# Performance work log

Measured on AMD Instinct MI355X. Metric: run time of the kernel, lower is better.

Reference implementation:

```python
import jax, jax.numpy as jnp
import numpy as np

N_HEADS = 32
N_KV_HEADS = 8
HEAD_DIM = 64
ROPE_BASE = 10000.0


def setup_inputs() -> dict:
    key = jax.random.key(0)
    ks = jax.random.split(key, 5)
    B, T, C = 4, 1024, 2048
    kv_dim = N_KV_HEADS * HEAD_DIM
    scale = 0.02
    return {
        "x": jax.random.normal(ks[0], (B, T, C), dtype=jnp.float32),
        "Wq": jax.random.normal(ks[1], (C, C), dtype=jnp.float32) * scale,
        "Wk": jax.random.normal(ks[2], (C, kv_dim), dtype=jnp.float32) * scale,
        "Wv": jax.random.normal(ks[3], (C, kv_dim), dtype=jnp.float32) * scale,
        "Wp": jax.random.normal(ks[4], (C, C), dtype=jnp.float32) * scale,
    }


def _rotate_half(x):
    # interleaved rotation: (x0,x1,x2,x3,...) -> (-x1,x0,-x3,x2,...)
    x1 = x[..., ::2]
    x2 = x[..., 1::2]
    return jnp.stack((-x2, x1), axis=-1).reshape(x.shape)


def _rope_tables(T, dtype):
    inv_freq = 1.0 / (ROPE_BASE ** (jnp.arange(0, HEAD_DIM, 2, dtype=jnp.float32) / HEAD_DIM))
    freqs = jnp.arange(T, dtype=jnp.float32)[:, None] * inv_freq[None, :]  # (T, D/2)
    cos = jnp.repeat(jnp.cos(freqs), 2, axis=-1).astype(dtype)  # (T, D)
    sin = jnp.repeat(jnp.sin(freqs), 2, axis=-1).astype(dtype)
    return cos[None, None], sin[None, None]  # (1,1,T,D)


def reference(x, Wq, Wk, Wv, Wp):
    B, T, C = x.shape
    H, KV, D = N_HEADS, N_KV_HEADS, HEAD_DIM
    q = (x @ Wq).reshape(B, T, H, D).transpose(0, 2, 1, 3)   # (B,H,T,D)
    k = (x @ Wk).reshape(B, T, KV, D).transpose(0, 2, 1, 3)  # (B,KV,T,D)
    v = (x @ Wv).reshape(B, T, KV, D).transpose(0, 2, 1, 3)

    cos, sin = _rope_tables(T, x.dtype)
    q = q * cos + _rotate_half(q) * sin
    k = k * cos + _rotate_half(k) * sin

    rf = H // KV
    k = jnp.repeat(k, rf, axis=1)  # (B,H,T,D) GQA broadcast
    v = jnp.repeat(v, rf, axis=1)

    scores = jnp.einsum('bhqd,bhkd->bhqk', q, k) / jnp.sqrt(jnp.asarray(D, x.dtype))
    causal = jnp.tril(jnp.ones((T, T), dtype=bool))
    scores = jnp.where(causal[None, None], scores, -jnp.inf)
    attn = jax.nn.softmax(scores, axis=-1)
    out = jnp.einsum('bhqk,bhkd->bhqd', attn, v)  # (B,H,T,D)
    out = out.transpose(0, 2, 1, 3).reshape(B, T, C)
    return out @ Wp
```

## Files before the change

kernel.cpp:

```cpp
#include <hip/hip_runtime.h>
#include <hip/hip_bf16.h>


typedef __attribute__((ext_vector_type(4))) float f32x4;
typedef __attribute__((ext_vector_type(8))) short short8;

#define AS1C(p) ((const __attribute__((address_space(1))) void*)(p))
#define AS3(p)  ((__attribute__((address_space(3))) void*)(p))

__device__ __forceinline__ unsigned short f2bf(float f) {
  union { float f; unsigned int u; } x; x.f = f;
  unsigned int r = x.u + 0x7FFFu + ((x.u >> 16) & 1u);
  return (unsigned short)(r >> 16);
}

__device__ __forceinline__ unsigned short bfc(float f) {
  return __bfloat16_as_ushort(__float2bfloat16(f));
}

__device__ __forceinline__ float ex2(float x) {
  return __builtin_amdgcn_exp2f(x);
}

__global__ void rope_tab_kernel(float2* __restrict__ tab) {
  const int idx = blockIdx.x * 256 + threadIdx.x;
  const int t = idx >> 5, i = idx & 31;
  const float invf = exp2f(-(float)i * 0.41524101186092029f);
  float sv, cv;
  __sincosf((float)t * invf, &sv, &cv);
  tab[idx] = make_float2(cv, sv);
}

__global__ void cvt_bf16_kernel(const float* __restrict__ src,
                                unsigned short* __restrict__ dst, int n4) {
  int i = blockIdx.x * blockDim.x + threadIdx.x;
  if (i >= n4) return;
  const f32x4 v = *(const f32x4*)(src + (size_t)i * 4);
  ushort4 u = make_ushort4(f2bf(v[0]), f2bf(v[1]), f2bf(v[2]), f2bf(v[3]));
  *(ushort4*)(dst + (size_t)i * 4) = u;
}

__global__ void transpose_qkv_w_kernel(const float* __restrict__ Wq,
                                       const float* __restrict__ Wk,
                                       const float* __restrict__ Wv,
                                       unsigned short* __restrict__ dst) {
  __shared__ float tile[32][33];
  const int z = blockIdx.z;
  const float* src;
  int N, rowOff;
  float scale;
  if (z == 0)      { src = Wq; N = 2048; rowOff = 0;    scale = 0.18033688011112042f; }
  else if (z == 1) { src = Wk; N = 512;  rowOff = 2048; scale = 1.0f; }
  else             { src = Wv; N = 512;  rowOff = 2560; scale = 1.0f; }
  const int n0 = blockIdx.x * 32, k0 = blockIdx.y * 32;
  if (n0 >= N) return;
  const int tx = threadIdx.x & 31, ty = threadIdx.x >> 5;
#pragma unroll
  for (int i = ty; i < 32; i += 8)
    tile[i][tx] = src[(size_t)(k0 + i) * N + (n0 + tx)];
  __syncthreads();
#pragma unroll
  for (int i = ty; i < 32; i += 8)
    dst[(size_t)(rowOff + n0 + i) * 2048 + (k0 + tx)] = f2bf(tile[tx][i] * scale);
}

__global__ void transpose_bf16_kernel(const float* __restrict__ src,
                                      unsigned short* __restrict__ dst,
                                      int N, int rowOff, float scale) {
  __shared__ float tile[32][33];
  const int n0 = blockIdx.x * 32, k0 = blockIdx.y * 32;
  const int tx = threadIdx.x & 31, ty = threadIdx.x >> 5;
#pragma unroll
  for (int i = ty; i < 32; i += 8)
    tile[i][tx] = src[(size_t)(k0 + i) * N + (n0 + tx)];
  __syncthreads();
#pragma unroll
  for (int i = ty; i < 32; i += 8)
    dst[(size_t)(rowOff + n0 + i) * 2048 + (k0 + tx)] = f2bf(tile[tx][i] * scale);
}

__global__ void rope_cvt2_kernel(const float2* __restrict__ tab,
                                 const float* __restrict__ qkf,
                                 unsigned short* __restrict__ qb,
                                 unsigned short* __restrict__ kb) {
  const int idx = blockIdx.x * 256 + threadIdx.x;
  const int m = idx / 320;
  const int p = idx - m * 320;
  const int t = m & 1023;
  unsigned short* dst;
  int srcCol, dcol;
  if (p < 256) { dcol = p * 8; srcCol = dcol; dst = qb + (size_t)m * 2048 + dcol; }
  else         { dcol = (p - 256) * 8; srcCol = 2048 + dcol; dst = kb + (size_t)m * 512 + dcol; }
  const int i0 = (srcCol & 63) >> 1;
  const float* src = qkf + (size_t)m * 2560 + srcCol;
  const f32x4 v0 = *(const f32x4*)(src);
  const f32x4 v1 = *(const f32x4*)(src + 4);
  float x[8] = {v0[0], v0[1], v0[2], v0[3], v1[0], v1[1], v1[2], v1[3]};
  short8 o;
#pragma unroll
  for (int j = 0; j < 4; ++j) {
    const float2 cs = tab[t * 32 + i0 + j];
    const float x1 = x[2 * j], x2 = x[2 * j + 1];
    o[2 * j]     = (short)bfc(x1 * cs.x - x2 * cs.y);
    o[2 * j + 1] = (short)bfc(x2 * cs.x + x1 * cs.y);
  }
  *(short8*)dst = o;
}

#define BAR() __builtin_amdgcn_s_barrier()

#define SA3(tile, half)                                                                  \
  do {                                                                                   \
    const unsigned short* p_ = Ap + (size_t)(m0 + (half) * 128 + sr) * 2048 + (tile) * 64 + sc; \
    const int d_ = (((tile) & 1) << 14) + ((half) << 13) + tid * 8;                      \
    __builtin_amdgcn_global_load_lds(AS1C(p_), AS3(&S[d_]), 16, 0, 0);                   \
    __builtin_amdgcn_global_load_lds(AS1C(p_ + (size_t)64 * 2048), AS3(&S[d_ + 4096]), 16, 0, 0); \
  } while (0)

#define SB3(tile, u)                                                                     \
  do {                                                                                   \
    const unsigned short* p_ = Bp + (size_t)(n0 + (u) * 64 + sr) * 2048 + (tile) * 64 + sc; \
    const int d_ = 32768 + ((tile) & 1) * 12288 + (u) * 4096 + tid * 8;                  \
    __builtin_amdgcn_global_load_lds(AS1C(p_), AS3(&S[d_]), 16, 0, 0);                   \
  } while (0)

#define RDA3(tile)                                                                       \
  _Pragma("unroll") for (int kk = 0; kk < 2; ++kk)                                       \
  _Pragma("unroll") for (int fm = 0; fm < 4; ++fm) {                                     \
    const int r_ = mg * 64 + fm * 16 + l15;                                              \
    af[kk][fm] = *(const short8*)&S[(((tile) & 1) << 14) + r_ * 64 +                     \
                                    (((kk << 2) | lg) ^ (r_ & 7)) * 8];                  \
  }

#define RDB3(tile, p)                                                                    \
  _Pragma("unroll") for (int kk = 0; kk < 2; ++kk)                                       \
  _Pragma("unroll") for (int jj = 0; jj < 2; ++jj) {                                     \
    const int r_ = ng * 96 + ((p) * 2 + jj) * 16 + l15;                                  \
    bf[kk][jj] = *(const short8*)&S[32768 + ((tile) & 1) * 12288 + r_ * 64 +             \
                                    (((kk << 2) | lg) ^ (r_ & 7)) * 8];                  \
  }

#define MM3(p)                                                                           \
  do {                                                                                   \
    __builtin_amdgcn_s_setprio(1);                                                       \
    _Pragma("unroll") for (int kk = 0; kk < 2; ++kk)                                     \
    _Pragma("unroll") for (int fm = 0; fm < 4; ++fm)                                     \
    _Pragma("unroll") for (int jj = 0; jj < 2; ++jj)                                     \
      acc[fm][(p) * 2 + jj] = __builtin_amdgcn_mfma_f32_16x16x32_bf16(                   \
          af[kk][fm], bf[kk][jj], acc[fm][(p) * 2 + jj], 0, 0, 0);                       \
    __builtin_amdgcn_s_setprio(0);                                                       \
  } while (0)

__global__ __launch_bounds__(512, 1) void gemm256x192_qkv_kernel(
    const unsigned short* __restrict__ Ap, const unsigned short* __restrict__ Bp,
    float* __restrict__ qkf, unsigned short* __restrict__ vt) {
  __shared__ unsigned short S[57344];
  const int tid = threadIdx.x;
  const int lane = tid & 63, w = tid >> 6;
  const int l15 = lane & 15, lg = lane >> 4;
  int lid = blockIdx.x + 16 * blockIdx.y;
  lid = (lid & 7) * 32 + (lid >> 3);
  const int m0 = (lid >> 4) * 256, n0 = (lid & 15) * 192;
  const int mg = w >> 1;
  const int ng = w & 1;
  const int sr = tid >> 3;
  const int sc = ((tid & 7) ^ (sr & 7)) << 3;
  const int NT = 32;

  f32x4 acc[4][6];
#pragma unroll
  for (int i = 0; i < 4; ++i)
#pragma unroll
    for (int j = 0; j < 6; ++j)
#pragma unroll
      for (int c = 0; c < 4; ++c) acc[i][j][c] = 0.f;

  SA3(0, 0); SA3(0, 1); SB3(0, 0); SB3(0, 1); SB3(0, 2);
  SA3(1, 0); SA3(1, 1); SB3(1, 0);
  asm volatile("s_waitcnt vmcnt(5)" ::: "memory");
  BAR();

  short8 af[2][4], bf[2][2];

  for (int t = 0; t < NT; t += 2) {
    const bool nl = (t + 2 < NT);
    RDA3(t); RDB3(t, 0);
    SB3(t + 1, 1); SB3(t + 1, 2);
    BAR();
    MM3(0);
    BAR();
    RDB3(t, 1);
    if (nl) SA3(t + 2, 0);
    BAR();
    MM3(1);
    BAR();
    RDB3(t, 2);
    if (nl) {
      SA3(t + 2, 1); SB3(t + 2, 0);
      asm volatile("s_waitcnt vmcnt(5)" ::: "memory");
    } else {
      asm volatile("s_waitcnt vmcnt(0)" ::: "memory");
    }
    BAR();
    MM3(2);
    BAR();
    RDA3(t + 1); RDB3(t + 1, 0);
    if (nl) { SB3(t + 2, 1); SB3(t + 2, 2); }
    BAR();
    MM3(0);
    BAR();
    RDB3(t + 1, 1);
    if (nl) SA3(t + 3, 0);
    BAR();
    MM3(1);
    BAR();
    RDB3(t + 1, 2);
    if (nl) {
      SA3(t + 3, 1); SB3(t + 3, 0);
      asm volatile("s_waitcnt vmcnt(5)" ::: "memory");
    }
    BAR();
    MM3(2);
    BAR();
  }

#pragma unroll
  for (int fn = 0; fn < 6; ++fn) {
    const int col16 = n0 + ng * 96 + fn * 16;
    if (col16 < 2560) {
#pragma unroll
      for (int fm = 0; fm < 4; ++fm) {
        const int row = m0 + mg * 64 + fm * 16 + lg * 4;
        const size_t base = (size_t)row * 2560 + col16 + l15;
#pragma unroll
        for (int r = 0; r < 4; ++r) qkf[base + (size_t)r * 2560] = acc[fm][fn][r];
      }
    } else {
      const int dz = (col16 - 2560) >> 6;
      const int d = ((col16 - 2560) & 63) + l15;
#pragma unroll
      for (int fm = 0; fm < 4; ++fm) {
        const int row = m0 + mg * 64 + fm * 16 + lg * 4;
        const int z = (row >> 10) * 8 + dz;
        const int t0 = row & 1023;
        ushort4 u = make_ushort4(bfc(acc[fm][fn][0]), bfc(acc[fm][fn][1]),
                                 bfc(acc[fm][fn][2]), bfc(acc[fm][fn][3]));
        *(ushort4*)&vt[(size_t)z * 65536 + d * 1024 + t0] = u;
      }
    }
  }
}

#define SA2(tile, half)                                                                  \
  do {                                                                                   \
    const unsigned short* p_ = Ap + (size_t)(m0 + (half) * 128 + sr) * Kd + (tile) * 64 + sc; \
    const int d_ = (((tile) & 1) << 14) + ((half) << 13) + tid * 8;                      \
    __builtin_amdgcn_global_load_lds(AS1C(p_), AS3(&S[d_]), 16, 0, 0);                   \
    __builtin_amdgcn_global_load_lds(AS1C(p_ + (size_t)64 * Kd), AS3(&S[d_ + 4096]), 16, 0, 0); \
  } while (0)

#define SB2(tile)                                                                        \
  do {                                                                                   \
    const unsigned short* p_ = Bp + (size_t)(n0 + sr) * Kd + (tile) * 64 + sc;           \
    const int d_ = 32768 + (((tile) & 1) << 13) + tid * 8;                               \
    __builtin_amdgcn_global_load_lds(AS1C(p_), AS3(&S[d_]), 16, 0, 0);                   \
    __builtin_amdgcn_global_load_lds(AS1C(p_ + (size_t)64 * Kd), AS3(&S[d_ + 4096]), 16, 0, 0); \
  } while (0)

#define RDA2(tile, Msub)                                                                 \
  _Pragma("unroll") for (int kk = 0; kk < 2; ++kk)                                       \
  _Pragma("unroll") for (int fm = 0; fm < 4; ++fm) {                                     \
    const int r_ = (Msub) * 64 + fm * 16 + l15;                                          \
    af[kk][fm] = *(const short8*)&S[(((tile) & 1) << 14) + (ah << 13) + r_ * 64 +        \
                                    (((kk << 2) | lg) ^ (r_ & 7)) * 8];                  \
  }

#define RDB2(dst, tile)                                                                  \
  _Pragma("unroll") for (int kk = 0; kk < 2; ++kk)                                       \
  _Pragma("unroll") for (int j = 0; j < 2; ++j) {                                        \
    const int r_ = wn + j * 16 + l15;                                                    \
    dst[kk][j] = *(const short8*)&S[32768 + (((tile) & 1) << 13) + r_ * 64 +             \
                                    (((kk << 2) | lg) ^ (r_ & 7)) * 8];                  \
  }

#define MM2(Msub, bb)                                                                    \
  do {                                                                                   \
    __builtin_amdgcn_s_setprio(1);                                                       \
    _Pragma("unroll") for (int kk = 0; kk < 2; ++kk)                                     \
    _Pragma("unroll") for (int fm = 0; fm < 4; ++fm)                                     \
    _Pragma("unroll") for (int j = 0; j < 2; ++j)                                        \
      acc[(Msub) * 4 + fm][j] = __builtin_amdgcn_mfma_f32_16x16x32_bf16(                 \
          af[kk][fm], bb[kk][j], acc[(Msub) * 4 + fm][j], 0, 0, 0);                      \
    __builtin_amdgcn_s_setprio(0);                                                       \
  } while (0)

__global__ __launch_bounds__(512, 1) void gemm256x128_kernel(
    const unsigned short* __restrict__ Ap, const unsigned short* __restrict__ Bp,
    float* __restrict__ C, int K, int N) {
  __shared__ unsigned short S[49152];
  const int tid = threadIdx.x;
  const int lane = tid & 63, w = tid >> 6;
  const int l15 = lane & 15, lg = lane >> 4;
  const int nwgx = gridDim.x;
  const int nwg = nwgx * gridDim.y;
  int lid = blockIdx.x + nwgx * blockIdx.y;
  lid = (lid & 7) * (nwg >> 3) + (lid >> 3);
  const int m0 = (lid / nwgx) * 256, n0 = (lid % nwgx) * 128;
  const int ah = w >> 2;
  const int wn = (w & 3) * 32;
  const int NT = K >> 6;
  const int Kd = K;
  const int sr = tid >> 3;
  const int sc = ((tid & 7) ^ (sr & 7)) << 3;

  f32x4 acc[8][2];
#pragma unroll
  for (int i = 0; i < 8; ++i)
#pragma unroll
    for (int j = 0; j < 2; ++j)
#pragma unroll
      for (int c = 0; c < 4; ++c) acc[i][j][c] = 0.f;

  SB2(0); SA2(0, 0); SA2(0, 1); SB2(1); SA2(1, 0);
  asm volatile("s_waitcnt vmcnt(4)" ::: "memory");
  __builtin_amdgcn_s_barrier();

  short8 af[2][4], b0[2][2], b1[2][2];

  for (int t = 0; t < NT; t += 2) {
    const bool nl = (t + 2 < NT);
    RDA2(t, 0); RDB2(b0, t);
    SA2(t + 1, 1);
    BAR();
    MM2(0, b0);
    BAR();
    RDA2(t, 1);
    if (nl) {
      SB2(t + 2); SA2(t + 2, 0);
      asm volatile("s_waitcnt vmcnt(4)" ::: "memory");
    } else {
      asm volatile("s_waitcnt vmcnt(0)" ::: "memory");
    }
    BAR();
    MM2(1, b0);
    BAR();
    RDA2(t + 1, 0); RDB2(b1, t + 1);
    if (nl) SA2(t + 2, 1);
    BAR();
    MM2(0, b1);
    BAR();
    RDA2(t + 1, 1);
    if (nl) {
      SB2(t + 3); SA2(t + 3, 0);
      asm volatile("s_waitcnt vmcnt(4)" ::: "memory");
    }
    BAR();
    MM2(1, b1);
    BAR();
  }

#pragma unroll
  for (int fm8 = 0; fm8 < 8; ++fm8)
#pragma unroll
    for (int j = 0; j < 2; ++j) {
      const size_t base =
          (size_t)(m0 + ah * 128 + (fm8 >> 2) * 64 + (fm8 & 3) * 16 + lg * 4) * N +
          (n0 + wn + j * 16 + l15);
#pragma unroll
      for (int r = 0; r < 4; ++r) C[base + (size_t)r * N] = acc[fm8][j][r];
    }
}

__global__ __launch_bounds__(256) void attn_mfma_kernel(
    const unsigned short* __restrict__ qb, const unsigned short* __restrict__ kb,
    const unsigned short* __restrict__ vt, unsigned short* __restrict__ attnb) {
  int lid = blockIdx.x + 8 * (blockIdx.y + 32 * blockIdx.z);
  lid = (lid & 7) * 128 + (lid >> 3);
  const int bx = lid & 7, h = (lid >> 3) & 31, b = lid >> 8;
  const int kvh = h >> 2;
  __shared__ unsigned short S[20480];
  const int tid = threadIdx.x, lane = tid & 63, w = tid >> 6;
  const int l15 = lane & 15, lg = lane >> 4;
  const int rowbase = w * 16 + lg * 4;

  const int gi0 = w * 64 + lane;
  const int r0 = gi0 >> 3, g0 = (gi0 & 7) ^ (r0 & 7);
  const int gi1 = (4 + w) * 64 + lane;
  const int r1 = gi1 >> 3, g1 = (gi1 & 7) ^ (r1 & 7);

  const unsigned short* kbase = kb + (size_t)b * 1024 * 512 + kvh * 64;
  const unsigned short* vbase = vt + (size_t)(b * 8 + kvh) * 64 * 1024;

#define STAGE_KV(kOff, vOff, jj)                                                    \
  do {                                                                              \
    __builtin_amdgcn_global_load_lds(AS1C(kbase + ((jj) * 64 + r0) * 512 + g0 * 8), \
                                     AS3(&S[(kOff) + w * 512]), 16, 0, 0);          \
    __builtin_amdgcn_global_load_lds(AS1C(kbase + ((jj) * 64 + r1) * 512 + g1 * 8), \
                                     AS3(&S[(kOff) + (4 + w) * 512]), 16, 0, 0);    \
    __builtin_amdgcn_global_load_lds(AS1C(vbase + r0 * 1024 + (jj) * 64 + g0 * 8),  \
                                     AS3(&S[(vOff) + w * 512]), 16, 0, 0);          \
    __builtin_amdgcn_global_load_lds(AS1C(vbase + r1 * 1024 + (jj) * 64 + g1 * 8),  \
                                     AS3(&S[(vOff) + (4 + w) * 512]), 16, 0, 0);    \
  } while (0)

#define STAGE_Q(qt)                                                                     \
  do {                                                                                  \
    const size_t qr_ = (size_t)b * 1024 + (qt) * 64;                                    \
    __builtin_amdgcn_global_load_lds(AS1C(qb + (qr_ + r0) * 2048 + h * 64 + g0 * 8),    \
                                     AS3(&S[w * 512]), 16, 0, 0);                       \
    __builtin_amdgcn_global_load_lds(AS1C(qb + (qr_ + r1) * 2048 + h * 64 + g1 * 8),    \
                                     AS3(&S[(4 + w) * 512]), 16, 0, 0);                 \
  } while (0)

  const int qts0 = bx, qts1 = 15 - bx;

  short8 ones;
#pragma unroll
  for (int i = 0; i < 8; ++i) ones[i] = (short)0x3F80;

  STAGE_Q(qts0);
  STAGE_KV(4096, 12288, 0);
  __syncthreads();

  int g = 0;
  for (int sub = 0; sub < 2; ++sub) {
    const int qtc = sub ? qts1 : qts0;
    const size_t qrow0 = (size_t)b * 1024 + qtc * 64;

    short8 qf[2];
#pragma unroll
    for (int kk = 0; kk < 2; ++kk) {
      const int r = w * 16 + l15;
      const int gq = ((kk << 2) | lg) ^ (r & 7);
      qf[kk] = *(const short8*)&S[r * 64 + gq * 8];
    }

    f32x4 oa[4], oe;
#pragma unroll
    for (int r = 0; r < 4; ++r) oe[r] = 0.f;
#pragma unroll
    for (int fd = 0; fd < 4; ++fd)
#pragma unroll
      for (int r = 0; r < 4; ++r) oa[fd][r] = 0.f;

    for (int j = 0; j <= qtc; ++j, ++g) {
      const int cur = g & 1;
      const int kOff = 4096 + cur * 4096;
      const int vOff = 12288 + cur * 4096;
      if (g < 16) {
        const int nj = (g + 1 <= qts0) ? g + 1 : g - qts0;
        STAGE_KV(4096 + (cur ^ 1) * 4096, 12288 + (cur ^ 1) * 4096, nj);
      }

      f32x4 sa[4];
#pragma unroll
      for (int fn = 0; fn < 4; ++fn)
#pragma unroll
        for (int r = 0; r < 4; ++r) sa[fn][r] = 0.f;
#pragma unroll
      for (int kk = 0; kk < 2; ++kk) {
        short8 kf[4];
#pragma unroll
        for (int fn = 0; fn < 4; ++fn) {
          const int rkv = fn * 16 + l15;
          const int gk = ((kk << 2) | lg) ^ (rkv & 7);
          kf[fn] = *(const short8*)&S[kOff + rkv * 64 + gk * 8];
        }
        __builtin_amdgcn_s_setprio(1);
#pragma unroll
        for (int fn = 0; fn < 4; ++fn)
          sa[fn] = __builtin_amdgcn_mfma_f32_16x16x32_bf16(qf[kk], kf[fn], sa[fn], 0, 0, 0);
        __builtin_amdgcn_s_setprio(0);
      }

      if (j == qtc) {
#pragma unroll
        for (int r = 0; r < 4; ++r) {
          const int row = rowbase + r;
#pragma unroll
          for (int fn = 0; fn < 4; ++fn)
            if ((fn * 16 + l15) > row) sa[fn][r] = -INFINITY;
        }
      }
#pragma unroll
      for (int fn = 0; fn < 4; ++fn)
#pragma unroll
        for (int r = 0; r < 4; ++r) sa[fn][r] = ex2(sa[fn][r]);

#pragma unroll
      for (int r = 0; r < 4; ++r) {
        const int prow = rowbase + r;
#pragma unroll
        for (int fn = 0; fn < 4; ++fn) {
          const int col = fn * 16 + l15;
          const int gp = (col >> 3) ^ (prow & 7);
          S[prow * 64 + gp * 8 + (col & 7)] = bfc(sa[fn][r]);
        }
      }

#pragma unroll
      for (int kk = 0; kk < 2; ++kk) {
        const int rp = w * 16 + l15;
        const int gp = ((kk << 2) | lg) ^ (rp & 7);
        const short8 pf = *(const short8*)&S[rp * 64 + gp * 8];
        short8 vf[4];
#pragma unroll
        for (int fd = 0; fd < 4; ++fd) {
          const int rd = fd * 16 + l15;
          const int gv = ((kk << 2) | lg) ^ (rd & 7);
          vf[fd] = *(const short8*)&S[vOff + rd * 64 + gv * 8];
        }
        __builtin_amdgcn_s_setprio(1);
#pragma unroll
        for (int fd = 0; fd < 4; ++fd)
          oa[fd] = __builtin_amdgcn_mfma_f32_16x16x32_bf16(pf, vf[fd], oa[fd], 0, 0, 0);
        oe = __builtin_amdgcn_mfma_f32_16x16x32_bf16(pf, ones, oe, 0, 0, 0);
        __builtin_amdgcn_s_setprio(0);
      }

      __syncthreads();
    }

#pragma unroll
    for (int r = 0; r < 4; ++r) {
      const float inv = 1.0f / oe[r];
      const size_t row = qrow0 + rowbase + r;
#pragma unroll
      for (int fd = 0; fd < 4; ++fd)
        attnb[row * 2048 + h * 64 + fd * 16 + l15] = f2bf(oa[fd][r] * inv);
    }

    if (sub == 0) {
      STAGE_Q(qts1);
      __syncthreads();
    }
  }
#undef STAGE_KV
#undef STAGE_Q
}

extern "C" void kernel_launch(void* const* d_in, const int* in_sizes, int n_in,
                              void* d_out, int out_size, void* d_ws, size_t ws_size,
                              hipStream_t stream) {
  (void)in_sizes; (void)n_in; (void)out_size; (void)ws_size;
  const float* x  = (const float*)d_in[0];
  const float* Wq = (const float*)d_in[1];
  const float* Wk = (const float*)d_in[2];
  const float* Wv = (const float*)d_in[3];
  const float* Wp = (const float*)d_in[4];

  char* w = (char*)d_ws;
  unsigned short* xb    = (unsigned short*)(w);
  unsigned short* Wt    = (unsigned short*)(w + 16777216);
  unsigned short* Wpt   = (unsigned short*)(w + 29360128);
  float*          qkf   = (float*)(w + 37748736);
  unsigned short* vtb   = (unsigned short*)(w + 79691776);
  unsigned short* attnb = (unsigned short*)(w + 83886080);
  float2*         rtab  = (float2*)(w + 100663296);
  unsigned short* qb    = (unsigned short*)(w);
  unsigned short* kbuf  = (unsigned short*)(w + 16777216);
  float* out = (float*)d_out;

  rope_tab_kernel<<<128, 256, 0, stream>>>(rtab);
  cvt_bf16_kernel<<<8192, 256, 0, stream>>>(x, xb, 2097152);
  transpose_qkv_w_kernel<<<dim3(64, 64, 3), 256, 0, stream>>>(Wq, Wk, Wv, Wt);
  transpose_bf16_kernel<<<dim3(64, 64), 256, 0, stream>>>(Wp, Wpt, 2048, 0, 1.0f);

  gemm256x192_qkv_kernel<<<dim3(16, 16), 512, 0, stream>>>(xb, Wt, qkf, vtb);
  rope_cvt2_kernel<<<5120, 256, 0, stream>>>(rtab, qkf, qb, kbuf);
  attn_mfma_kernel<<<dim3(8, 32, 4), 256, 0, stream>>>(qb, kbuf, vtb, attnb);
  gemm256x128_kernel<<<dim3(16, 16), 512, 0, stream>>>(attnb, Wpt, out, 2048, 2048);
}
```

Before: 166.2 us.

## Triple-buffer B tiles in QKV GEMM and merge weight transpose launches

The QKV GEMM's B-operand LDS staging moves from double to triple buffering, so B loads for tile t+2 can be issued earlier and the vmcnt waits are relaxed to 7 outstanding loads. This is meant to hide more global-load latency behind the MFMA work, at the cost of extra LDS (about 136KB per block). Separately, the Wq/Wk/Wv and Wp transpose-convert kernels are merged into one launch with a z dimension of 4, removing one kernel launch.

```diff
diff --git a/kernel.cpp b/kernel.cpp
--- a/kernel.cpp
+++ b/kernel.cpp
@@ -40,35 +40,24 @@
   *(ushort4*)(dst + (size_t)i * 4) = u;
 }
 
-__global__ void transpose_qkv_w_kernel(const float* __restrict__ Wq,
-                                       const float* __restrict__ Wk,
-                                       const float* __restrict__ Wv,
-                                       unsigned short* __restrict__ dst) {
+__global__ void transpose_w_kernel(const float* __restrict__ Wq,
+                                   const float* __restrict__ Wk,
+                                   const float* __restrict__ Wv,
+                                   const float* __restrict__ Wp,
+                                   unsigned short* __restrict__ Wt,
+                                   unsigned short* __restrict__ Wpt) {
   __shared__ float tile[32][33];
   const int z = blockIdx.z;
   const float* src;
+  unsigned short* dst;
   int N, rowOff;
-  float scale;
-  if (z == 0)      { src = Wq; N = 2048; rowOff = 0;    scale = 0.18033688011112042f; }
-  else if (z == 1) { src = Wk; N = 512;  rowOff = 2048; scale = 1.0f; }
-  else             { src = Wv; N = 512;  rowOff = 2560; scale = 1.0f; }
+  float scale = 1.0f;
+  if (z == 0)      { src = Wq; dst = Wt;  N = 2048; rowOff = 0;    scale = 0.18033688011112042f; }
+  else if (z == 1) { src = Wk; dst = Wt;  N = 512;  rowOff = 2048; }
+  else if (z == 2) { src = Wv; dst = Wt;  N = 512;  rowOff = 2560; }
+  else             { src = Wp; dst = Wpt; N = 2048; rowOff = 0;    }
   const int n0 = blockIdx.x * 32, k0 = blockIdx.y * 32;
   if (n0 >= N) return;
-  const int tx = threadIdx.x & 31, ty = threadIdx.x >> 5;
-#pragma unroll
-  for (int i = ty; i < 32; i += 8)
-    tile[i][tx] = src[(size_t)(k0 + i) * N + (n0 + tx)];
-  __syncthreads();
-#pragma unroll
-  for (int i = ty; i < 32; i += 8)
-    dst[(size_t)(rowOff + n0 + i) * 2048 + (k0 + tx)] = f2bf(tile[tx][i] * scale);
-}
-
-__global__ void transpose_bf16_kernel(const float* __restrict__ src,
-                                      unsigned short* __restrict__ dst,
-                                      int N, int rowOff, float scale) {
-  __shared__ float tile[32][33];
-  const int n0 = blockIdx.x * 32, k0 = blockIdx.y * 32;
   const int tx = threadIdx.x & 31, ty = threadIdx.x >> 5;
 #pragma unroll
   for (int i = ty; i < 32; i += 8)
@@ -120,7 +109,7 @@
 #define SB3(tile, u)                                                                     \
   do {                                                                                   \
     const unsigned short* p_ = Bp + (size_t)(n0 + (u) * 64 + sr) * 2048 + (tile) * 64 + sc; \
-    const int d_ = 32768 + ((tile) & 1) * 12288 + (u) * 4096 + tid * 8;                  \
+    const int d_ = 32768 + ((tile) % 3) * 12288 + (u) * 4096 + tid * 8;                  \
     __builtin_amdgcn_global_load_lds(AS1C(p_), AS3(&S[d_]), 16, 0, 0);                   \
   } while (0)
 
@@ -136,7 +125,7 @@
   _Pragma("unroll") for (int kk = 0; kk < 2; ++kk)                                       \
   _Pragma("unroll") for (int jj = 0; jj < 2; ++jj) {                                     \
     const int r_ = ng * 96 + ((p) * 2 + jj) * 16 + l15;                                  \
-    bf[kk][jj] = *(const short8*)&S[32768 + ((tile) & 1) * 12288 + r_ * 64 +             \
+    bf[kk][jj] = *(const short8*)&S[32768 + ((tile) % 3) * 12288 + r_ * 64 +             \
                                     (((kk << 2) | lg) ^ (r_ & 7)) * 8];                  \
   }
 
@@ -154,7 +143,7 @@
 __global__ __launch_bounds__(512, 1) void gemm256x192_qkv_kernel(
     const unsigned short* __restrict__ Ap, const unsigned short* __restrict__ Bp,
     float* __restrict__ qkf, unsigned short* __restrict__ vt) {
-  __shared__ unsigned short S[57344];
+  __shared__ unsigned short S[69632];
   const int tid = threadIdx.x;
   const int lane = tid & 63, w = tid >> 6;
   const int l15 = lane & 15, lg = lane >> 4;
@@ -175,9 +164,9 @@
 #pragma unroll
       for (int c = 0; c < 4; ++c) acc[i][j][c] = 0.f;
 
-  SA3(0, 0); SA3(0, 1); SB3(0, 0); SB3(0, 1); SB3(0, 2);
-  SA3(1, 0); SA3(1, 1); SB3(1, 0);
-  asm volatile("s_waitcnt vmcnt(5)" ::: "memory");
+  SB3(0, 0); SB3(0, 1); SB3(0, 2); SA3(0, 0); SA3(0, 1);
+  SB3(1, 0); SB3(1, 1); SB3(1, 2); SA3(1, 0); SA3(1, 1);
+  asm volatile("s_waitcnt vmcnt(7)" ::: "memory");
   BAR();
 
   short8 af[2][4], bf[2][2];
@@ -185,19 +174,19 @@
   for (int t = 0; t < NT; t += 2) {
     const bool nl = (t + 2 < NT);
     RDA3(t); RDB3(t, 0);
-    SB3(t + 1, 1); SB3(t + 1, 2);
+    if (nl) { SB3(t + 2, 0); SB3(t + 2, 1); }
     BAR();
     MM3(0);
     BAR();
     RDB3(t, 1);
-    if (nl) SA3(t + 2, 0);
+    if (nl) { SA3(t + 2, 0); SB3(t + 2, 2); }
     BAR();
     MM3(1);
     BAR();
     RDB3(t, 2);
     if (nl) {
-      SA3(t + 2, 1); SB3(t + 2, 0);
-      asm volatile("s_waitcnt vmcnt(5)" ::: "memory");
+      SA3(t + 2, 1);
+      asm volatile("s_waitcnt vmcnt(7)" ::: "memory");
     } else {
       asm volatile("s_waitcnt vmcnt(0)" ::: "memory");
     }
@@ -205,19 +194,19 @@
     MM3(2);
     BAR();
     RDA3(t + 1); RDB3(t + 1, 0);
-    if (nl) { SB3(t + 2, 1); SB3(t + 2, 2); }
+    if (nl) SB3(t + 3, 0);
     BAR();
     MM3(0);
     BAR();
     RDB3(t + 1, 1);
-    if (nl) SA3(t + 3, 0);
+    if (nl) { SA3(t + 3, 0); SB3(t + 3, 1); }
     BAR();
     MM3(1);
     BAR();
     RDB3(t + 1, 2);
     if (nl) {
-      SA3(t + 3, 1); SB3(t + 3, 0);
-      asm volatile("s_waitcnt vmcnt(5)" ::: "memory");
+      SA3(t + 3, 1); SB3(t + 3, 2);
+      asm volatile("s_waitcnt vmcnt(7)" ::: "memory");
     }
     BAR();
     MM3(2);
@@ -288,7 +277,7 @@
     __builtin_amdgcn_s_setprio(1);                                                       \
     _Pragma("unroll") for (int kk = 0; kk < 2; ++kk)                                     \
     _Pragma("unroll") for (int fm = 0; fm < 4; ++fm)                                     \
-    _Pragma("unroll") for (int j = 0; j < 2; ++j)                                        \
+    _Pragma("unroll") for (int j = 0; j < 2; ++j)                                       \
       acc[(Msub) * 4 + fm][j] = __builtin_amdgcn_mfma_f32_16x16x32_bf16(                 \
           af[kk][fm], bb[kk][j], acc[(Msub) * 4 + fm][j], 0, 0, 0);                      \
     __builtin_amdgcn_s_setprio(0);                                                       \
@@ -563,8 +552,7 @@
 
   rope_tab_kernel<<<128, 256, 0, stream>>>(rtab);
   cvt_bf16_kernel<<<8192, 256, 0, stream>>>(x, xb, 2097152);
-  transpose_qkv_w_kernel<<<dim3(64, 64, 3), 256, 0, stream>>>(Wq, Wk, Wv, Wt);
-  transpose_bf16_kernel<<<dim3(64, 64), 256, 0, stream>>>(Wp, Wpt, 2048, 0, 1.0f);
+  transpose_w_kernel<<<dim3(64, 64, 4), 256, 0, stream>>>(Wq, Wk, Wv, Wp, Wt, Wpt);
 
   gemm256x192_qkv_kernel<<<dim3(16, 16), 512, 0, stream>>>(xb, Wt, qkf, vtb);
   rope_cvt2_kernel<<<5120, 256, 0, stream>>>(rtab, qkf, qb, kbuf);
```

Result: no change. 166.3 us (+0.1%).
